# Kernel optimization log

Measured on AMD Instinct MI355X. Metric: run time of the kernel, lower is better.

Reference implementation:

```python
import jax, jax.numpy as jnp
import numpy as np

N_SRC = 100000
N_DST = 100000
E = 500000
D = 128      # in_units
F = 64       # efeat_dim
NB = 2       # num_basis
C = 5        # num_classes


def setup_inputs() -> dict:
    key = jax.random.key(0)
    ks = jax.random.split(key, 14)
    s = 1.0 / np.sqrt(D)
    return {
        "h_src": jax.random.normal(ks[0], (N_SRC, D), jnp.float32),
        "h_dst": jax.random.normal(ks[1], (N_DST, D), jnp.float32),
        "efeats": jax.random.normal(ks[2], (E, F), jnp.float32),
        "u_idx": jax.random.randint(ks[3], (E,), 0, N_SRC),
        "v_idx": jax.random.randint(ks[4], (E,), 0, N_DST),
        "W1": jax.random.normal(ks[5], (D, F), jnp.float32) * (1.0 / np.sqrt(F)),
        "b1": jnp.zeros((D,), jnp.float32),
        "W2": jax.random.normal(ks[6], (D, D), jnp.float32) * s,
        "b2": jnp.zeros((D,), jnp.float32),
        "W3": jax.random.normal(ks[7], (D, D), jnp.float32) * s,
        "b3": jnp.zeros((D,), jnp.float32),
        "W_comb": jax.random.normal(ks[8], (D, 2 * D), jnp.float32) * (1.0 / np.sqrt(2 * D)),
        "P": jax.random.normal(ks[9], (NB, D, D), jnp.float32) * s,
        "W_cb": jax.random.normal(ks[10], (C, NB), jnp.float32) * (1.0 / np.sqrt(NB)),
    }


def reference(h_src, h_dst, efeats, u_idx, v_idx,
              W1, b1, W2, b2, W3, b3, W_comb, P, W_cb):
    # 3-layer edge-feature MLP (dropout is identity at eval / rate=0)
    e = jax.nn.relu(efeats @ W1.T + b1)   # [E, D]
    e = jax.nn.relu(e @ W2.T + b2)        # [E, D]
    e = e @ W3.T + b3                     # [E, D]
    # gather node feats by edge endpoints, concat with transformed efeats, combine
    u = jnp.concatenate([h_src[u_idx], e], axis=1) @ W_comb.T  # [E, D]
    v = jnp.concatenate([h_dst[v_idx], e], axis=1) @ W_comb.T  # [E, D]
    # bilinear basis decode: out[e, b] = u[e] @ P[b] @ v[e]
    out = jnp.einsum('ei,bij,ej->eb', u, P, v)  # [E, NB]
    return out @ W_cb.T                          # [E, C]
```

## Files before the change

kernel.cpp:

```cpp
#include <hip/hip_runtime.h>

#define NNODE 100000
#define EDG   500000
#define DD    128
#define FF    64
#define NBAS  2
#define NCLS  5

#define OFF_B1   0
#define OFF_B2   8192
#define OFF_B3   24576
#define OFF_BCR  40960
#define OFF_BCL  57344
#define OFF_P0   73728
#define OFF_P1   90112
#define OFF_HU   106496
#define OFF_HV   (106496 + NNODE * DD)
#define PREP_TOT 106496

typedef __attribute__((ext_vector_type(8))) short short8;
typedef __attribute__((ext_vector_type(4))) float f32x4;

__device__ __forceinline__ float bf2f(ushort u) {
  return __uint_as_float(((unsigned int)u) << 16);
}
__device__ __forceinline__ ushort f2bf(float f) {
  unsigned int u = __float_as_uint(f);
  u += 0x7FFF + ((u >> 16) & 1);
  return (ushort)(u >> 16);
}

__device__ __forceinline__ void zacc(f32x4 a[4][2]) {
#pragma unroll
  for (int i = 0; i < 4; ++i)
#pragma unroll
    for (int j = 0; j < 2; ++j)
      a[i][j] = (f32x4){0.f, 0.f, 0.f, 0.f};
}

__device__ __forceinline__ void gemm_core(const ushort act[][136],
                                          const ushort* __restrict__ Bp,
                                          int ksteps, f32x4 acc[4][2],
                                          int w, int l15, int q) {
  for (int ks = 0; ks < ksteps; ++ks) {
    short8 bfrag[2], afrag[4];
#pragma unroll
    for (int c2 = 0; c2 < 2; ++c2) {
      int n = w * 32 + c2 * 16 + l15;
      bfrag[c2] = *(const short8*)(Bp + ((ks * 4 + q) * 128 + n) * 8);
    }
#pragma unroll
    for (int rt = 0; rt < 4; ++rt)
      afrag[rt] = *(const short8*)&act[rt * 16 + l15][ks * 32 + q * 8];
#pragma unroll
    for (int rt = 0; rt < 4; ++rt)
#pragma unroll
      for (int c2 = 0; c2 < 2; ++c2)
        acc[rt][c2] = __builtin_amdgcn_mfma_f32_16x16x32_bf16(
            afrag[rt], bfrag[c2], acc[rt][c2], 0, 0, 0);
  }
}

__device__ __forceinline__ void store_tiles(ushort dest[][136], f32x4 acc[4][2],
                                            const float* __restrict__ bias,
                                            int relu, int w, int l15, int q) {
#pragma unroll
  for (int rt = 0; rt < 4; ++rt)
#pragma unroll
    for (int c2 = 0; c2 < 2; ++c2) {
      int col = w * 32 + c2 * 16 + l15;
      float bv = bias ? bias[col] : 0.f;
#pragma unroll
      for (int r = 0; r < 4; ++r) {
        int row = rt * 16 + q * 4 + r;
        float v = acc[rt][c2][r] + bv;
        if (relu) v = fmaxf(v, 0.f);
        dest[row][col] = f2bf(v);
      }
    }
}

__global__ void __launch_bounds__(256) prep_kernel(
    const float* __restrict__ W1, const float* __restrict__ W2,
    const float* __restrict__ W3, const float* __restrict__ W_comb,
    const float* __restrict__ P, ushort* __restrict__ ws) {
  int idx = blockIdx.x * 256 + threadIdx.x;
  if (idx >= PREP_TOT) return;
  float val;
  if (idx < 8192) {
    int g = idx >> 10, n = (idx >> 3) & 127, j = idx & 7, k = g * 8 + j;
    val = W1[n * 64 + k];
  } else {
    int i2 = idx - 8192;
    int m = i2 >> 14, r = i2 & 16383;
    int g = r >> 10, n = (r >> 3) & 127, j = r & 7, k = g * 8 + j;
    switch (m) {
      case 0:  val = W2[n * 128 + k]; break;
      case 1:  val = W3[n * 128 + k]; break;
      case 2:  val = W_comb[n * 256 + 128 + k]; break;
      case 3:  val = W_comb[n * 256 + k]; break;
      case 4:  val = P[n * 128 + k]; break;
      default: val = P[16384 + n * 128 + k]; break;
    }
  }
  ws[idx] = f2bf(val);
}

__global__ void __launch_bounds__(256) node_kernel(
    const float* __restrict__ h_src, const float* __restrict__ h_dst,
    ushort* __restrict__ ws) {
  __shared__ ushort ACT[64][136];
  const int NT = (NNODE + 63) / 64;
  const int tid = threadIdx.x;
  const int w = tid >> 6, lane = tid & 63, l15 = lane & 15, q = lane >> 4;
  const int bb = blockIdx.x;
  const float* h = (bb < NT) ? h_src : h_dst;
  ushort* op = ws + ((bb < NT) ? OFF_HU : OFF_HV);
  const int tile = (bb < NT) ? bb : bb - NT;
  const int r0 = tile * 64;
  {
    const int r = tid >> 2, part = tid & 3;
    int row = r0 + r; if (row >= NNODE) row = NNODE - 1;
    const float4* src = (const float4*)(h + (long)row * DD) + part * 8;
    ushort* dst = &ACT[r][part * 32];
#pragma unroll
    for (int i = 0; i < 8; ++i) {
      float4 v = src[i];
      ushort4 hh; hh.x = f2bf(v.x); hh.y = f2bf(v.y);
      hh.z = f2bf(v.z); hh.w = f2bf(v.w);
      *(ushort4*)(dst + i * 4) = hh;
    }
  }
  __syncthreads();
  f32x4 acc[4][2];
  zacc(acc);
  gemm_core(ACT, ws + OFF_BCL, 4, acc, w, l15, q);
#pragma unroll
  for (int rt = 0; rt < 4; ++rt)
#pragma unroll
    for (int c2 = 0; c2 < 2; ++c2) {
      int col = w * 32 + c2 * 16 + l15;
#pragma unroll
      for (int r = 0; r < 4; ++r) {
        int row = r0 + rt * 16 + q * 4 + r;
        if (row < NNODE) op[(long)row * DD + col] = f2bf(acc[rt][c2][r]);
      }
    }
}

__global__ void __launch_bounds__(256) edge_kernel(
    const float* __restrict__ efeats, const int* __restrict__ u_idx,
    const int* __restrict__ v_idx, const float* __restrict__ b1,
    const float* __restrict__ b2, const float* __restrict__ b3,
    const float* __restrict__ W_cb, const ushort* __restrict__ ws,
    float* __restrict__ out) {
  __shared__ ushort ACT[64][136];
  __shared__ ushort EC[64][136];
  __shared__ float OB[64][2];

  const int tid = threadIdx.x;
  const int w = tid >> 6, lane = tid & 63;
  const int l15 = lane & 15, q = lane >> 4;
  const long e0 = (long)blockIdx.x * 64;

  {
    const int r = tid >> 2, part = tid & 3;
    long row = e0 + r; if (row >= EDG) row = EDG - 1;
    const float4* src = (const float4*)(efeats + row * FF) + part * 4;
    ushort* dst = &ACT[r][part * 16];
#pragma unroll
    for (int i = 0; i < 4; ++i) {
      float4 v = src[i];
      ushort4 hh; hh.x = f2bf(v.x); hh.y = f2bf(v.y);
      hh.z = f2bf(v.z); hh.w = f2bf(v.w);
      *(ushort4*)(dst + i * 4) = hh;
    }
  }
  __syncthreads();

  f32x4 acc[4][2];
  zacc(acc); gemm_core(ACT, ws + OFF_B1, 2, acc, w, l15, q);
  __syncthreads(); store_tiles(ACT, acc, b1, 1, w, l15, q); __syncthreads();
  zacc(acc); gemm_core(ACT, ws + OFF_B2, 4, acc, w, l15, q);
  __syncthreads(); store_tiles(ACT, acc, b2, 1, w, l15, q); __syncthreads();
  zacc(acc); gemm_core(ACT, ws + OFF_B3, 4, acc, w, l15, q);
  __syncthreads(); store_tiles(ACT, acc, b3, 0, w, l15, q); __syncthreads();
  zacc(acc); gemm_core(ACT, ws + OFF_BCR, 4, acc, w, l15, q);
  __syncthreads(); store_tiles(EC, acc, nullptr, 0, w, l15, q); __syncthreads();

  {
    const int r = tid >> 2, part = tid & 3;
    long row = e0 + r; if (row >= EDG) row = EDG - 1;
    const int vi = v_idx[row];
    const ushort* hp = ws + OFF_HV + (long)vi * DD + part * 32;
    const ushort* ep = &EC[r][part * 32];
    ushort* dst = &ACT[r][part * 32];
#pragma unroll
    for (int ch = 0; ch < 8; ++ch) {
      ushort4 a = *(const ushort4*)(hp + ch * 4);
      ushort4 b = *(const ushort4*)(ep + ch * 4);
      ushort4 o;
      o.x = f2bf(bf2f(a.x) + bf2f(b.x));
      o.y = f2bf(bf2f(a.y) + bf2f(b.y));
      o.z = f2bf(bf2f(a.z) + bf2f(b.z));
      o.w = f2bf(bf2f(a.w) + bf2f(b.w));
      *(ushort4*)(dst + ch * 4) = o;
    }
  }
  __syncthreads();

  f32x4 tacc[2][4][2];
  zacc(tacc[0]); zacc(tacc[1]);
  gemm_core(ACT, ws + OFF_P0, 4, tacc[0], w, l15, q);
  gemm_core(ACT, ws + OFF_P1, 4, tacc[1], w, l15, q);
  __syncthreads();

  {
    const int r = tid >> 2, part = tid & 3;
    long row = e0 + r; if (row >= EDG) row = EDG - 1;
    const int ui = u_idx[row];
    const ushort* hp = ws + OFF_HU + (long)ui * DD + part * 32;
    const ushort* ep = &EC[r][part * 32];
    ushort* dst = &ACT[r][part * 32];
#pragma unroll
    for (int ch = 0; ch < 8; ++ch) {
      ushort4 a = *(const ushort4*)(hp + ch * 4);
      ushort4 b = *(const ushort4*)(ep + ch * 4);
      ushort4 o;
      o.x = f2bf(bf2f(a.x) + bf2f(b.x));
      o.y = f2bf(bf2f(a.y) + bf2f(b.y));
      o.z = f2bf(bf2f(a.z) + bf2f(b.z));
      o.w = f2bf(bf2f(a.w) + bf2f(b.w));
      *(ushort4*)(dst + ch * 4) = o;
    }
    if (tid < 128) OB[tid >> 1][tid & 1] = 0.f;
  }
  __syncthreads();

#pragma unroll
  for (int b = 0; b < 2; ++b)
#pragma unroll
    for (int rt = 0; rt < 4; ++rt) {
      float p[4] = {0.f, 0.f, 0.f, 0.f};
#pragma unroll
      for (int c2 = 0; c2 < 2; ++c2) {
        int col = w * 32 + c2 * 16 + l15;
        int rbase = rt * 16 + q * 4;
#pragma unroll
        for (int r = 0; r < 4; ++r)
          p[r] += tacc[b][rt][c2][r] * bf2f(ACT[rbase + r][col]);
      }
#pragma unroll
      for (int m = 1; m < 16; m <<= 1) {
#pragma unroll
        for (int r = 0; r < 4; ++r) p[r] += __shfl_xor(p[r], m, 64);
      }
      if (l15 == 0) {
        int rbase = rt * 16 + q * 4;
#pragma unroll
        for (int r = 0; r < 4; ++r) atomicAdd(&OB[rbase + r][b], p[r]);
      }
    }
  __syncthreads();

  for (int t = tid; t < 64 * NCLS; t += 256) {
    int r = t / NCLS, c = t % NCLS;
    long erow = e0 + r;
    if (erow < EDG) {
      float o = OB[r][0] * W_cb[c * NBAS + 0] + OB[r][1] * W_cb[c * NBAS + 1];
      out[erow * NCLS + c] = o;
    }
  }
}

extern "C" void kernel_launch(void* const* d_in, const int* in_sizes, int n_in,
                              void* d_out, int out_size, void* d_ws,
                              size_t ws_size, hipStream_t stream) {
  const float* h_src  = (const float*)d_in[0];
  const float* h_dst  = (const float*)d_in[1];
  const float* efeats = (const float*)d_in[2];
  const int*   u_idx  = (const int*)d_in[3];
  const int*   v_idx  = (const int*)d_in[4];
  const float* W1     = (const float*)d_in[5];
  const float* b1     = (const float*)d_in[6];
  const float* W2     = (const float*)d_in[7];
  const float* b2     = (const float*)d_in[8];
  const float* W3     = (const float*)d_in[9];
  const float* b3     = (const float*)d_in[10];
  const float* W_comb = (const float*)d_in[11];
  const float* P      = (const float*)d_in[12];
  const float* W_cb   = (const float*)d_in[13];
  ushort* ws = (ushort*)d_ws;
  float* out = (float*)d_out;

  prep_kernel<<<(PREP_TOT + 255) / 256, 256, 0, stream>>>(W1, W2, W3, W_comb, P, ws);
  node_kernel<<<2 * ((NNODE + 63) / 64), 256, 0, stream>>>(h_src, h_dst, ws);
  edge_kernel<<<(EDG + 63) / 64, 256, 0, stream>>>(efeats, u_idx, v_idx,
                                                   b1, b2, b3, W_cb, ws, out);
}
```

Before: 511.9 us.

## Swap GEMM operand roles, enlarge edge tiles to 128, prefetch gathered node rows

```diff
diff --git a/kernel.cpp b/kernel.cpp
--- a/kernel.cpp
+++ b/kernel.cpp
@@ -4,14 +4,13 @@
 #define EDG   500000
 #define DD    128
 #define FF    64
-#define NBAS  2
 #define NCLS  5
 
-#define OFF_B1   0
-#define OFF_B2   8192
-#define OFF_B3   24576
-#define OFF_BCR  40960
-#define OFF_BCL  57344
+#define OFF_W1   0
+#define OFF_W2   8192
+#define OFF_W3   24576
+#define OFF_WCR  40960
+#define OFF_WCL  57344
 #define OFF_P0   73728
 #define OFF_P1   90112
 #define OFF_HU   106496
@@ -21,6 +20,8 @@
 typedef __attribute__((ext_vector_type(8))) short short8;
 typedef __attribute__((ext_vector_type(4))) float f32x4;
 
+union U4 { uint4 v; ushort s[8]; };
+
 __device__ __forceinline__ float bf2f(ushort u) {
   return __uint_as_float(((unsigned int)u) << 16);
 }
@@ -30,54 +31,51 @@
   return (ushort)(u >> 16);
 }
 
-__device__ __forceinline__ void zacc(f32x4 a[4][2]) {
-#pragma unroll
-  for (int i = 0; i < 4; ++i)
-#pragma unroll
-    for (int j = 0; j < 2; ++j)
+__device__ __forceinline__ void zacc(f32x4 a[2][4]) {
+#pragma unroll
+  for (int i = 0; i < 2; ++i)
+#pragma unroll
+    for (int j = 0; j < 4; ++j)
       a[i][j] = (f32x4){0.f, 0.f, 0.f, 0.f};
 }
 
-__device__ __forceinline__ void gemm_core(const ushort act[][136],
-                                          const ushort* __restrict__ Bp,
-                                          int ksteps, f32x4 acc[4][2],
-                                          int w, int l15, int q) {
+__device__ __forceinline__ void gemm_T(const ushort (*act)[136],
+                                       const ushort* __restrict__ W, int K,
+                                       int ksteps, f32x4 acc[2][4],
+                                       int m0, int n0, int l15, int q) {
   for (int ks = 0; ks < ksteps; ++ks) {
-    short8 bfrag[2], afrag[4];
-#pragma unroll
-    for (int c2 = 0; c2 < 2; ++c2) {
-      int n = w * 32 + c2 * 16 + l15;
-      bfrag[c2] = *(const short8*)(Bp + ((ks * 4 + q) * 128 + n) * 8);
-    }
-#pragma unroll
-    for (int rt = 0; rt < 4; ++rt)
-      afrag[rt] = *(const short8*)&act[rt * 16 + l15][ks * 32 + q * 8];
-#pragma unroll
-    for (int rt = 0; rt < 4; ++rt)
-#pragma unroll
-      for (int c2 = 0; c2 < 2; ++c2)
-        acc[rt][c2] = __builtin_amdgcn_mfma_f32_16x16x32_bf16(
-            afrag[rt], bfrag[c2], acc[rt][c2], 0, 0, 0);
-  }
-}
-
-__device__ __forceinline__ void store_tiles(ushort dest[][136], f32x4 acc[4][2],
-                                            const float* __restrict__ bias,
-                                            int relu, int w, int l15, int q) {
-#pragma unroll
-  for (int rt = 0; rt < 4; ++rt)
-#pragma unroll
-    for (int c2 = 0; c2 < 2; ++c2) {
-      int col = w * 32 + c2 * 16 + l15;
-      float bv = bias ? bias[col] : 0.f;
-#pragma unroll
-      for (int r = 0; r < 4; ++r) {
-        int row = rt * 16 + q * 4 + r;
-        float v = acc[rt][c2][r] + bv;
-        if (relu) v = fmaxf(v, 0.f);
-        dest[row][col] = f2bf(v);
+    const int ko = ks * 32 + q * 8;
+    short8 a0 = *(const short8*)(W + (m0 + l15) * K + ko);
+    short8 a1 = *(const short8*)(W + (m0 + 16 + l15) * K + ko);
+#pragma unroll
+    for (int nt = 0; nt < 4; ++nt) {
+      short8 b = *(const short8*)&act[n0 + nt * 16 + l15][ko];
+      acc[0][nt] = __builtin_amdgcn_mfma_f32_16x16x32_bf16(a0, b, acc[0][nt], 0, 0, 0);
+      acc[1][nt] = __builtin_amdgcn_mfma_f32_16x16x32_bf16(a1, b, acc[1][nt], 0, 0, 0);
+    }
+  }
+}
+
+__device__ __forceinline__ void store_T(ushort (*dst)[136], f32x4 acc[2][4],
+                                        const float* __restrict__ bias, int relu,
+                                        int m0, int n0, int l15, int q) {
+#pragma unroll
+  for (int mt = 0; mt < 2; ++mt) {
+    const int feat = m0 + mt * 16 + q * 4;
+    float4 bv = bias ? *(const float4*)(bias + feat) : make_float4(0.f, 0.f, 0.f, 0.f);
+#pragma unroll
+    for (int nt = 0; nt < 4; ++nt) {
+      const int edge = n0 + nt * 16 + l15;
+      float v0 = acc[mt][nt][0] + bv.x, v1 = acc[mt][nt][1] + bv.y;
+      float v2 = acc[mt][nt][2] + bv.z, v3 = acc[mt][nt][3] + bv.w;
+      if (relu) {
+        v0 = fmaxf(v0, 0.f); v1 = fmaxf(v1, 0.f);
+        v2 = fmaxf(v2, 0.f); v3 = fmaxf(v3, 0.f);
       }
-    }
+      ushort4 o; o.x = f2bf(v0); o.y = f2bf(v1); o.z = f2bf(v2); o.w = f2bf(v3);
+      *(ushort4*)&dst[edge][feat] = o;
+    }
+  }
 }
 
 __global__ void __launch_bounds__(256) prep_kernel(
@@ -88,187 +86,189 @@
   if (idx >= PREP_TOT) return;
   float val;
   if (idx < 8192) {
-    int g = idx >> 10, n = (idx >> 3) & 127, j = idx & 7, k = g * 8 + j;
-    val = W1[n * 64 + k];
+    val = W1[idx];
   } else {
-    int i2 = idx - 8192;
-    int m = i2 >> 14, r = i2 & 16383;
-    int g = r >> 10, n = (r >> 3) & 127, j = r & 7, k = g * 8 + j;
+    int r = idx - 8192, m = r >> 14, rr = r & 16383;
     switch (m) {
-      case 0:  val = W2[n * 128 + k]; break;
-      case 1:  val = W3[n * 128 + k]; break;
-      case 2:  val = W_comb[n * 256 + 128 + k]; break;
-      case 3:  val = W_comb[n * 256 + k]; break;
-      case 4:  val = P[n * 128 + k]; break;
-      default: val = P[16384 + n * 128 + k]; break;
+      case 0:  val = W2[rr]; break;
+      case 1:  val = W3[rr]; break;
+      case 2:  { int n = rr >> 7, k = rr & 127; val = W_comb[n * 256 + 128 + k]; } break;
+      case 3:  { int n = rr >> 7, k = rr & 127; val = W_comb[n * 256 + k]; } break;
+      case 4:  val = P[rr]; break;
+      default: val = P[16384 + rr]; break;
     }
   }
   ws[idx] = f2bf(val);
 }
 
-__global__ void __launch_bounds__(256) node_kernel(
+__global__ void __launch_bounds__(512, 4) node_kernel(
     const float* __restrict__ h_src, const float* __restrict__ h_dst,
     ushort* __restrict__ ws) {
-  __shared__ ushort ACT[64][136];
-  const int NT = (NNODE + 63) / 64;
+  __shared__ ushort ACT[128][136];
+  const int NT = (NNODE + 127) / 128;
   const int tid = threadIdx.x;
   const int w = tid >> 6, lane = tid & 63, l15 = lane & 15, q = lane >> 4;
+  const int m0 = (w & 3) * 32, n0 = (w >> 2) * 64;
   const int bb = blockIdx.x;
   const float* h = (bb < NT) ? h_src : h_dst;
   ushort* op = ws + ((bb < NT) ? OFF_HU : OFF_HV);
-  const int tile = (bb < NT) ? bb : bb - NT;
-  const int r0 = tile * 64;
-  {
-    const int r = tid >> 2, part = tid & 3;
-    int row = r0 + r; if (row >= NNODE) row = NNODE - 1;
+  const int r0 = ((bb < NT) ? bb : bb - NT) * 128;
+  const int srow = tid >> 2, part = tid & 3;
+  int row = r0 + srow; if (row >= NNODE) row = NNODE - 1;
+  {
     const float4* src = (const float4*)(h + (long)row * DD) + part * 8;
-    ushort* dst = &ACT[r][part * 32];
+    ushort* d = &ACT[srow][part * 32];
 #pragma unroll
     for (int i = 0; i < 8; ++i) {
       float4 v = src[i];
-      ushort4 hh; hh.x = f2bf(v.x); hh.y = f2bf(v.y);
-      hh.z = f2bf(v.z); hh.w = f2bf(v.w);
-      *(ushort4*)(dst + i * 4) = hh;
-    }
-  }
-  __syncthreads();
-  f32x4 acc[4][2];
+      ushort4 hh; hh.x = f2bf(v.x); hh.y = f2bf(v.y); hh.z = f2bf(v.z); hh.w = f2bf(v.w);
+      *(ushort4*)(d + i * 4) = hh;
+    }
+  }
+  __syncthreads();
+  f32x4 acc[2][4];
   zacc(acc);
-  gemm_core(ACT, ws + OFF_BCL, 4, acc, w, l15, q);
-#pragma unroll
-  for (int rt = 0; rt < 4; ++rt)
-#pragma unroll
-    for (int c2 = 0; c2 < 2; ++c2) {
-      int col = w * 32 + c2 * 16 + l15;
-#pragma unroll
-      for (int r = 0; r < 4; ++r) {
-        int row = r0 + rt * 16 + q * 4 + r;
-        if (row < NNODE) op[(long)row * DD + col] = f2bf(acc[rt][c2][r]);
-      }
-    }
-}
-
-__global__ void __launch_bounds__(256) edge_kernel(
+  gemm_T(ACT, ws + OFF_WCL, 128, 4, acc, m0, n0, l15, q);
+  __syncthreads();
+  store_T(ACT, acc, nullptr, 0, m0, n0, l15, q);
+  __syncthreads();
+  if (r0 + srow < NNODE) {
+    const uint4* s = (const uint4*)&ACT[srow][part * 32];
+    uint4* d = (uint4*)(op + (long)(r0 + srow) * DD + part * 32);
+#pragma unroll
+    for (int i = 0; i < 4; ++i) d[i] = s[i];
+  }
+}
+
+__global__ void __launch_bounds__(512, 4) edge_kernel(
     const float* __restrict__ efeats, const int* __restrict__ u_idx,
     const int* __restrict__ v_idx, const float* __restrict__ b1,
     const float* __restrict__ b2, const float* __restrict__ b3,
     const float* __restrict__ W_cb, const ushort* __restrict__ ws,
     float* __restrict__ out) {
-  __shared__ ushort ACT[64][136];
-  __shared__ ushort EC[64][136];
-  __shared__ float OB[64][2];
+  __shared__ ushort ACT[128][136];
+  __shared__ ushort EC[128][136];
+  __shared__ float OB[128][2];
 
   const int tid = threadIdx.x;
   const int w = tid >> 6, lane = tid & 63;
   const int l15 = lane & 15, q = lane >> 4;
-  const long e0 = (long)blockIdx.x * 64;
-
-  {
-    const int r = tid >> 2, part = tid & 3;
-    long row = e0 + r; if (row >= EDG) row = EDG - 1;
-    const float4* src = (const float4*)(efeats + row * FF) + part * 4;
-    ushort* dst = &ACT[r][part * 16];
+  const int m0 = (w & 3) * 32, n0 = (w >> 2) * 64;
+  const long e0 = (long)blockIdx.x * 128;
+
+  const int srow = tid >> 2, part = tid & 3;
+  long grow = e0 + srow; if (grow >= EDG) grow = EDG - 1;
+  const int vi = v_idx[grow], ui = u_idx[grow];
+
+  {
+    const float4* src = (const float4*)(efeats + grow * FF) + part * 4;
+    ushort* d = &ACT[srow][part * 16];
 #pragma unroll
     for (int i = 0; i < 4; ++i) {
       float4 v = src[i];
-      ushort4 hh; hh.x = f2bf(v.x); hh.y = f2bf(v.y);
-      hh.z = f2bf(v.z); hh.w = f2bf(v.w);
-      *(ushort4*)(dst + i * 4) = hh;
-    }
-  }
-  __syncthreads();
-
-  f32x4 acc[4][2];
-  zacc(acc); gemm_core(ACT, ws + OFF_B1, 2, acc, w, l15, q);
-  __syncthreads(); store_tiles(ACT, acc, b1, 1, w, l15, q); __syncthreads();
-  zacc(acc); gemm_core(ACT, ws + OFF_B2, 4, acc, w, l15, q);
-  __syncthreads(); store_tiles(ACT, acc, b2, 1, w, l15, q); __syncthreads();
-  zacc(acc); gemm_core(ACT, ws + OFF_B3, 4, acc, w, l15, q);
-  __syncthreads(); store_tiles(ACT, acc, b3, 0, w, l15, q); __syncthreads();
-  zacc(acc); gemm_core(ACT, ws + OFF_BCR, 4, acc, w, l15, q);
-  __syncthreads(); store_tiles(EC, acc, nullptr, 0, w, l15, q); __syncthreads();
-
-  {
-    const int r = tid >> 2, part = tid & 3;
-    long row = e0 + r; if (row >= EDG) row = EDG - 1;
-    const int vi = v_idx[row];
-    const ushort* hp = ws + OFF_HV + (long)vi * DD + part * 32;
-    const ushort* ep = &EC[r][part * 32];
-    ushort* dst = &ACT[r][part * 32];
-#pragma unroll
-    for (int ch = 0; ch < 8; ++ch) {
-      ushort4 a = *(const ushort4*)(hp + ch * 4);
-      ushort4 b = *(const ushort4*)(ep + ch * 4);
-      ushort4 o;
-      o.x = f2bf(bf2f(a.x) + bf2f(b.x));
-      o.y = f2bf(bf2f(a.y) + bf2f(b.y));
-      o.z = f2bf(bf2f(a.z) + bf2f(b.z));
-      o.w = f2bf(bf2f(a.w) + bf2f(b.w));
-      *(ushort4*)(dst + ch * 4) = o;
-    }
-  }
-  __syncthreads();
-
-  f32x4 tacc[2][4][2];
+      ushort4 hh; hh.x = f2bf(v.x); hh.y = f2bf(v.y); hh.z = f2bf(v.z); hh.w = f2bf(v.w);
+      *(ushort4*)(d + i * 4) = hh;
+    }
+  }
+  __syncthreads();
+
+  f32x4 acc[2][4];
+  zacc(acc); gemm_T(ACT, ws + OFF_W1, 64, 2, acc, m0, n0, l15, q);
+  __syncthreads(); store_T(ACT, acc, b1, 1, m0, n0, l15, q); __syncthreads();
+  zacc(acc); gemm_T(ACT, ws + OFF_W2, 128, 4, acc, m0, n0, l15, q);
+  __syncthreads(); store_T(ACT, acc, b2, 1, m0, n0, l15, q); __syncthreads();
+  zacc(acc); gemm_T(ACT, ws + OFF_W3, 128, 4, acc, m0, n0, l15, q);
+  __syncthreads(); store_T(ACT, acc, b3, 0, m0, n0, l15, q); __syncthreads();
+
+  uint4 hvp[4];
+  {
+    const uint4* hp = (const uint4*)(ws + OFF_HV + (long)vi * DD + part * 32);
+#pragma unroll
+    for (int c = 0; c < 4; ++c) hvp[c] = hp[c];
+  }
+  zacc(acc); gemm_T(ACT, ws + OFF_WCR, 128, 4, acc, m0, n0, l15, q);
+  __syncthreads(); store_T(EC, acc, nullptr, 0, m0, n0, l15, q); __syncthreads();
+
+  {
+#pragma unroll
+    for (int c = 0; c < 4; ++c) {
+      U4 a; a.v = hvp[c];
+      U4 e; e.v = *(const uint4*)&EC[srow][part * 32 + c * 8];
+      U4 o;
+#pragma unroll
+      for (int j = 0; j < 8; ++j) o.s[j] = f2bf(bf2f(a.s[j]) + bf2f(e.s[j]));
+      *(uint4*)&ACT[srow][part * 32 + c * 8] = o.v;
+    }
+    if (tid < 256) OB[tid >> 1][tid & 1] = 0.f;
+  }
+  __syncthreads();
+
+  uint4 hup[4];
+  {
+    const uint4* hp = (const uint4*)(ws + OFF_HU + (long)ui * DD + part * 32);
+#pragma unroll
+    for (int c = 0; c < 4; ++c) hup[c] = hp[c];
+  }
+
+  f32x4 tacc[2][2][4];
   zacc(tacc[0]); zacc(tacc[1]);
-  gemm_core(ACT, ws + OFF_P0, 4, tacc[0], w, l15, q);
-  gemm_core(ACT, ws + OFF_P1, 4, tacc[1], w, l15, q);
-  __syncthreads();
-
-  {
-    const int r = tid >> 2, part = tid & 3;
-    long row = e0 + r; if (row >= EDG) row = EDG - 1;
-    const int ui = u_idx[row];
-    const ushort* hp = ws + OFF_HU + (long)ui * DD + part * 32;
-    const ushort* ep = &EC[r][part * 32];
-    ushort* dst = &ACT[r][part * 32];
-#pragma unroll
-    for (int ch = 0; ch < 8; ++ch) {
-      ushort4 a = *(const ushort4*)(hp + ch * 4);
-      ushort4 b = *(const ushort4*)(ep + ch * 4);
-      ushort4 o;
-      o.x = f2bf(bf2f(a.x) + bf2f(b.x));
-      o.y = f2bf(bf2f(a.y) + bf2f(b.y));
-      o.z = f2bf(bf2f(a.z) + bf2f(b.z));
-      o.w = f2bf(bf2f(a.w) + bf2f(b.w));
-      *(ushort4*)(dst + ch * 4) = o;
-    }
-    if (tid < 128) OB[tid >> 1][tid & 1] = 0.f;
-  }
-  __syncthreads();
-
-#pragma unroll
-  for (int b = 0; b < 2; ++b)
-#pragma unroll
-    for (int rt = 0; rt < 4; ++rt) {
-      float p[4] = {0.f, 0.f, 0.f, 0.f};
-#pragma unroll
-      for (int c2 = 0; c2 < 2; ++c2) {
-        int col = w * 32 + c2 * 16 + l15;
-        int rbase = rt * 16 + q * 4;
-#pragma unroll
-        for (int r = 0; r < 4; ++r)
-          p[r] += tacc[b][rt][c2][r] * bf2f(ACT[rbase + r][col]);
-      }
-#pragma unroll
-      for (int m = 1; m < 16; m <<= 1) {
-#pragma unroll
-        for (int r = 0; r < 4; ++r) p[r] += __shfl_xor(p[r], m, 64);
-      }
-      if (l15 == 0) {
-        int rbase = rt * 16 + q * 4;
-#pragma unroll
-        for (int r = 0; r < 4; ++r) atomicAdd(&OB[rbase + r][b], p[r]);
-      }
-    }
-  __syncthreads();
-
-  for (int t = tid; t < 64 * NCLS; t += 256) {
+  for (int ks = 0; ks < 4; ++ks) {
+    const int ko = ks * 32 + q * 8;
+    short8 a00 = *(const short8*)(ws + OFF_P0 + (m0 + l15) * 128 + ko);
+    short8 a01 = *(const short8*)(ws + OFF_P0 + (m0 + 16 + l15) * 128 + ko);
+    short8 a10 = *(const short8*)(ws + OFF_P1 + (m0 + l15) * 128 + ko);
+    short8 a11 = *(const short8*)(ws + OFF_P1 + (m0 + 16 + l15) * 128 + ko);
+#pragma unroll
+    for (int nt = 0; nt < 4; ++nt) {
+      short8 b = *(const short8*)&ACT[n0 + nt * 16 + l15][ko];
+      tacc[0][0][nt] = __builtin_amdgcn_mfma_f32_16x16x32_bf16(a00, b, tacc[0][0][nt], 0, 0, 0);
+      tacc[0][1][nt] = __builtin_amdgcn_mfma_f32_16x16x32_bf16(a01, b, tacc[0][1][nt], 0, 0, 0);
+      tacc[1][0][nt] = __builtin_amdgcn_mfma_f32_16x16x32_bf16(a10, b, tacc[1][0][nt], 0, 0, 0);
+      tacc[1][1][nt] = __builtin_amdgcn_mfma_f32_16x16x32_bf16(a11, b, tacc[1][1][nt], 0, 0, 0);
+    }
+  }
+  __syncthreads();
+
+  {
+#pragma unroll
+    for (int c = 0; c < 4; ++c) {
+      U4 a; a.v = hup[c];
+      U4 e; e.v = *(const uint4*)&EC[srow][part * 32 + c * 8];
+      U4 o;
+#pragma unroll
+      for (int j = 0; j < 8; ++j) o.s[j] = f2bf(bf2f(a.s[j]) + bf2f(e.s[j]));
+      *(uint4*)&ACT[srow][part * 32 + c * 8] = o.v;
+    }
+  }
+  __syncthreads();
+
+#pragma unroll
+  for (int nt = 0; nt < 4; ++nt) {
+    const int edge = n0 + nt * 16 + l15;
+    float pb0 = 0.f, pb1 = 0.f;
+#pragma unroll
+    for (int mt = 0; mt < 2; ++mt) {
+      ushort4 u4 = *(const ushort4*)&ACT[edge][m0 + mt * 16 + q * 4];
+      float uf;
+      uf = bf2f(u4.x); pb0 += tacc[0][mt][nt][0] * uf; pb1 += tacc[1][mt][nt][0] * uf;
+      uf = bf2f(u4.y); pb0 += tacc[0][mt][nt][1] * uf; pb1 += tacc[1][mt][nt][1] * uf;
+      uf = bf2f(u4.z); pb0 += tacc[0][mt][nt][2] * uf; pb1 += tacc[1][mt][nt][2] * uf;
+      uf = bf2f(u4.w); pb0 += tacc[0][mt][nt][3] * uf; pb1 += tacc[1][mt][nt][3] * uf;
+    }
+    pb0 += __shfl_xor(pb0, 16, 64); pb0 += __shfl_xor(pb0, 32, 64);
+    pb1 += __shfl_xor(pb1, 16, 64); pb1 += __shfl_xor(pb1, 32, 64);
+    if (q == 0) {
+      atomicAdd(&OB[edge][0], pb0);
+      atomicAdd(&OB[edge][1], pb1);
+    }
+  }
+  __syncthreads();
+
+  for (int t = tid; t < 128 * NCLS; t += 512) {
     int r = t / NCLS, c = t % NCLS;
     long erow = e0 + r;
     if (erow < EDG) {
-      float o = OB[r][0] * W_cb[c * NBAS + 0] + OB[r][1] * W_cb[c * NBAS + 1];
-      out[erow * NCLS + c] = o;
+      out[erow * NCLS + c] = OB[r][0] * W_cb[c * 2] + OB[r][1] * W_cb[c * 2 + 1];
     }
   }
 }
@@ -294,7 +294,7 @@
   float* out = (float*)d_out;
 
   prep_kernel<<<(PREP_TOT + 255) / 256, 256, 0, stream>>>(W1, W2, W3, W_comb, P, ws);
-  node_kernel<<<2 * ((NNODE + 63) / 64), 256, 0, stream>>>(h_src, h_dst, ws);
-  edge_kernel<<<(EDG + 63) / 64, 256, 0, stream>>>(efeats, u_idx, v_idx,
-                                                   b1, b2, b3, W_cb, ws, out);
-}
+  node_kernel<<<2 * ((NNODE + 127) / 128), 512, 0, stream>>>(h_src, h_dst, ws);
+  edge_kernel<<<(EDG + 127) / 128, 512, 0, stream>>>(efeats, u_idx, v_idx,
+                                                     b1, b2, b3, W_cb, ws, out);
+}
```

Result: no change. 503.7 us (-1.6%).
